# Optimization experiments

Hardware: AMD Instinct MI355X
Metric: run time of the kernel (lower is better)

Reference implementation:

```python
import jax, jax.numpy as jnp
import numpy as np

N_NODES = 100000
N_EDGES = 1600000
IN_DIM = 32
OUT_DIM = 64
N_REL = 8
EPS = 1e-10


def setup_inputs() -> dict:
    key = jax.random.key(0)
    k_x, k_src, k_dst, k_rel, k_w, k_wl, k_ws = jax.random.split(key, 7)
    x = jax.random.normal(k_x, (N_NODES, IN_DIM), dtype=jnp.float32)
    node_in = jax.random.randint(k_src, (N_EDGES,), 0, N_NODES)
    node_out = jax.random.randint(k_dst, (N_EDGES,), 0, N_NODES)
    relation = jax.random.randint(k_rel, (N_EDGES,), 0, N_REL)
    edge_list = jnp.stack([node_in, node_out, relation], axis=1)  # [E, 3] int
    edge_weight = jax.random.uniform(k_w, (N_EDGES,), dtype=jnp.float32)
    W_linear = jax.random.normal(k_wl, (N_REL * IN_DIM, OUT_DIM), dtype=jnp.float32) / np.sqrt(N_REL * IN_DIM)
    b_linear = jnp.zeros((OUT_DIM,), dtype=jnp.float32)
    W_self = jax.random.normal(k_ws, (IN_DIM, OUT_DIM), dtype=jnp.float32) / np.sqrt(IN_DIM)
    b_self = jnp.zeros((OUT_DIM,), dtype=jnp.float32)
    return {"x": x, "edge_list": edge_list, "edge_weight": edge_weight,
            "W_linear": W_linear, "b_linear": b_linear,
            "W_self": W_self, "b_self": b_self}


def reference(x, edge_list, edge_weight, W_linear, b_linear, W_self, b_self):
    num_node, in_dim = x.shape
    # message: gather source-node features per edge  -> [E, D]
    msg = x[edge_list[:, 0]]
    # aggregate: relation-expanded segment id = dst * R + rel
    seg = edge_list[:, 1] * N_REL + edge_list[:, 2]  # [E]
    w = edge_weight[:, None]  # [E, 1]
    num = jax.ops.segment_sum(msg * w, seg, num_segments=num_node * N_REL)  # [N*R, D]
    den = jax.ops.segment_sum(w, seg, num_segments=num_node * N_REL)        # [N*R, 1]
    update = (num / (den + EPS)).reshape(num_node, N_REL * in_dim)          # [N, R*D]
    # combine: linear(update) + self_loop(x), then ReLU
    out = update @ W_linear + b_linear + x @ W_self + b_self
    return jax.nn.relu(out)
```

## Files before the change

kernel.cpp:

```cpp
#include <hip/hip_runtime.h>
#include <stdint.h>

#define N_NODES 100000
#define N_EDGES 1600000
#define IN_DIM 32
#define OUT_DIM 64
#define N_REL 8
#define NSEG (N_NODES * N_REL)
#define EPS 1e-10f
#define N_KK 9
#define SWG_ELEMS (N_KK * 4 * 64 * 8)

#define SCAN_ELEMS 4096
#define SCAN_NB ((NSEG + SCAN_ELEMS - 1) / SCAN_ELEMS)

#define N_XCD 8
#define NODES_PER_SLICE (N_NODES / N_XCD)

typedef __attribute__((ext_vector_type(8))) short bf16x8;
typedef __attribute__((ext_vector_type(4))) float f32x4;

static __device__ __forceinline__ float bflo(uint32_t u) { return __uint_as_float(u << 16); }
static __device__ __forceinline__ float bfhi(uint32_t u) { return __uint_as_float(u & 0xffff0000u); }
static __device__ __forceinline__ uint16_t f2bf(float f) {
    uint32_t u = __float_as_uint(f);
    return (uint16_t)((u + 0x7fffu + ((u >> 16) & 1u)) >> 16);
}

__global__ __launch_bounds__(256) void detect_kernel(const uint32_t* __restrict__ xw,
                                                     int* __restrict__ flag) {
    __shared__ int cnt;
    if (threadIdx.x == 0) cnt = 0;
    __syncthreads();
    int c = 0;
    for (int k = threadIdx.x; k < 4096; k += 256) {
        uint32_t w = xw[k];
        uint32_t e = (w >> 7) & 0xffu;
        c += (e >= 160u) ? 1 : 0;
    }
    atomicAdd(&cnt, c);
    __syncthreads();
    if (threadIdx.x == 0) *flag = (cnt > 64) ? 1 : 0;
}

__global__ __launch_bounds__(256) void prep_kernel(const void* __restrict__ Wl,
                                                   const void* __restrict__ Ws,
                                                   const void* __restrict__ bl,
                                                   const void* __restrict__ bs,
                                                   const int* __restrict__ flag,
                                                   uint16_t* __restrict__ sWg,
                                                   float* __restrict__ biasv) {
    int f32 = *flag;
    int idx = blockIdx.x * 256 + threadIdx.x;
    if (idx < SWG_ELEMS) {
        int j    = idx & 7;
        int lane = (idx >> 3) & 63;
        int ot   = (idx >> 9) & 3;
        int kk   = idx >> 11;
        int quad = lane >> 4;
        int k = kk * 32 + quad * 8 + j;
        int o = ot * 16 + (lane & 15);
        if (f32) {
            float v = (k < 256) ? ((const float*)Wl)[(size_t)k * OUT_DIM + o]
                                : ((const float*)Ws)[(size_t)(k - 256) * OUT_DIM + o];
            sWg[idx] = f2bf(v);
        } else {
            sWg[idx] = (k < 256) ? ((const uint16_t*)Wl)[(size_t)k * OUT_DIM + o]
                                 : ((const uint16_t*)Ws)[(size_t)(k - 256) * OUT_DIM + o];
        }
    } else if (idx < SWG_ELEMS + OUT_DIM) {
        int o = idx - SWG_ELEMS;
        if (f32) biasv[o] = ((const float*)bl)[o] + ((const float*)bs)[o];
        else     biasv[o] = bflo((uint32_t)((const uint16_t*)bl)[o])
                          + bflo((uint32_t)((const uint16_t*)bs)[o]);
    }
}

__global__ __launch_bounds__(256) void xbf_kernel(const void* __restrict__ x,
                                                  const int* __restrict__ flag,
                                                  uint16_t* __restrict__ xbf) {
    int i = blockIdx.x * 256 + threadIdx.x;
    if (i >= N_NODES * IN_DIM / 8) return;
    if (*flag) {
        const float4 v0 = ((const float4*)x)[(size_t)i * 2];
        const float4 v1 = ((const float4*)x)[(size_t)i * 2 + 1];
        bf16x8 r;
        r[0] = (short)f2bf(v0.x); r[1] = (short)f2bf(v0.y);
        r[2] = (short)f2bf(v0.z); r[3] = (short)f2bf(v0.w);
        r[4] = (short)f2bf(v1.x); r[5] = (short)f2bf(v1.y);
        r[6] = (short)f2bf(v1.z); r[7] = (short)f2bf(v1.w);
        *(bf16x8*)(xbf + (size_t)i * 8) = r;
    } else {
        *(bf16x8*)(xbf + (size_t)i * 8) = ((const bf16x8*)x)[i];
    }
}

__global__ __launch_bounds__(256) void hist_kernel(const int* __restrict__ el,
                                                   uint32_t* __restrict__ cnt) {
    int e = blockIdx.x * 256 + threadIdx.x;
    if (e >= N_EDGES) return;
    int dst = el[e * 3 + 1];
    int rel = el[e * 3 + 2];
    atomicAdd(&cnt[dst * N_REL + rel], 1u);
}

__global__ __launch_bounds__(256) void scan1_kernel(const uint32_t* __restrict__ cnt,
                                                    uint32_t* __restrict__ bsum) {
    int base = blockIdx.x * SCAN_ELEMS + threadIdx.x * 16;
    uint32_t s = 0;
    #pragma unroll
    for (int j = 0; j < 16; ++j) {
        int i = base + j;
        s += (i < NSEG) ? cnt[i] : 0u;
    }
    __shared__ uint32_t ls[256];
    ls[threadIdx.x] = s;
    __syncthreads();
    #pragma unroll
    for (int off = 128; off > 0; off >>= 1) {
        if (threadIdx.x < off) ls[threadIdx.x] += ls[threadIdx.x + off];
        __syncthreads();
    }
    if (threadIdx.x == 0) bsum[blockIdx.x] = ls[0];
}

__global__ __launch_bounds__(256) void scan2_kernel(uint32_t* __restrict__ bsum) {
    __shared__ uint32_t ls[256];
    int tid = threadIdx.x;
    ls[tid] = (tid < SCAN_NB) ? bsum[tid] : 0u;
    __syncthreads();
    if (tid == 0) {
        uint32_t run = 0;
        for (int i = 0; i < SCAN_NB; ++i) { uint32_t c = ls[i]; ls[i] = run; run += c; }
    }
    __syncthreads();
    if (tid < SCAN_NB) bsum[tid] = ls[tid];
}

__global__ __launch_bounds__(256) void scan3_kernel(const uint32_t* __restrict__ bsum,
                                                    uint32_t* __restrict__ ptr,
                                                    uint32_t* __restrict__ cursor) {
    int tid = threadIdx.x;
    int base = blockIdx.x * SCAN_ELEMS + tid * 16;
    uint32_t v[16];
    uint32_t run = 0;
    #pragma unroll
    for (int j = 0; j < 16; ++j) {
        int i = base + j;
        uint32_t c = (i < NSEG) ? cursor[i] : 0u;
        v[j] = run;
        run += c;
    }
    __shared__ uint32_t ls[256];
    ls[tid] = run;
    __syncthreads();
    for (int off = 1; off < 256; off <<= 1) {
        uint32_t t = (tid >= off) ? ls[tid - off] : 0u;
        __syncthreads();
        ls[tid] += t;
        __syncthreads();
    }
    uint32_t texcl = ls[tid] - run;
    uint32_t boff = bsum[blockIdx.x];
    #pragma unroll
    for (int j = 0; j < 16; ++j) {
        int i = base + j;
        if (i < NSEG) {
            uint32_t val = boff + texcl + v[j];
            ptr[i]    = val;
            cursor[i] = val;
        }
    }
    if (blockIdx.x == 0 && tid == 0) ptr[NSEG] = N_EDGES;
}

__global__ __launch_bounds__(256) void sort_kernel(const int* __restrict__ el,
                                                   const void* __restrict__ ew,
                                                   const int* __restrict__ flag,
                                                   uint32_t* __restrict__ cursor,
                                                   uint2* __restrict__ sorted) {
    int b = blockIdx.x;
    int tile  = b >> 3;
    int slice = b & 7;
    int e = tile * 256 + threadIdx.x;
    if (e >= N_EDGES) return;
    int dst = el[e * 3 + 1];
    if (dst / NODES_PER_SLICE != slice) return;
    int src = el[e * 3 + 0];
    int rel = el[e * 3 + 2];
    float w = (*flag) ? ((const float*)ew)[e]
                      : bflo((uint32_t)((const uint16_t*)ew)[e]);
    int seg = dst * N_REL + rel;
    uint32_t pos = atomicAdd(&cursor[seg], 1u);
    sorted[pos] = make_uint2((uint32_t)src, __float_as_uint(w));
}

__global__ __launch_bounds__(256) void fused_dense_kernel(
    const uint32_t* __restrict__ ptr,
    const uint2* __restrict__ sorted,
    const uint16_t* __restrict__ xbf,
    const uint16_t* __restrict__ sWg,
    const float* __restrict__ biasv,
    const int* __restrict__ flag,
    void* __restrict__ out)
{
    __shared__ uint16_t sB[SWG_ELEMS];
    int f32 = *flag;

    #pragma unroll
    for (int it = 0; it < SWG_ELEMS / (256 * 8); ++it) {
        int idx = (it * 256 + threadIdx.x) * 8;
        *(bf16x8*)(sB + idx) = *(const bf16x8*)(sWg + idx);
    }
    __syncthreads();

    int wid  = threadIdx.x >> 6;
    int lane = threadIdx.x & 63;
    int quad = lane >> 4;
    int m    = lane & 15;

    int n0 = blockIdx.x * 64 + wid * 16;
    int n  = n0 + m;
    int nc = (n < N_NODES) ? n : (N_NODES - 1);

    float bias[4];
    #pragma unroll
    for (int ot = 0; ot < 4; ++ot) bias[ot] = biasv[ot * 16 + m];

    f32x4 acc[4];
    #pragma unroll
    for (int ot = 0; ot < 4; ++ot) acc[ot] = (f32x4){0.f, 0.f, 0.f, 0.f};

    #pragma unroll
    for (int kk = 0; kk < N_KK; ++kk) {
        bf16x8 a;
        if (kk < 8) {
            int seg = nc * N_REL + kk;
            int beg = (int)ptr[seg];
            int end = (int)ptr[seg + 1];
            float s0 = 0.f, s1 = 0.f, s2 = 0.f, s3 = 0.f;
            float s4 = 0.f, s5 = 0.f, s6 = 0.f, s7 = 0.f, sw = 0.f;
            for (int i = beg; i < end; ++i) {
                uint2 d = sorted[i];
                float w = __uint_as_float(d.y);
                const uint4 xv = *(const uint4*)(xbf + (size_t)d.x * IN_DIM + quad * 8);
                s0 += w * bflo(xv.x); s1 += w * bfhi(xv.x);
                s2 += w * bflo(xv.y); s3 += w * bfhi(xv.y);
                s4 += w * bflo(xv.z); s5 += w * bfhi(xv.z);
                s6 += w * bflo(xv.w); s7 += w * bfhi(xv.w);
                sw += w;
            }
            float inv = 1.0f / (sw + EPS);
            a[0] = (short)f2bf(s0 * inv); a[1] = (short)f2bf(s1 * inv);
            a[2] = (short)f2bf(s2 * inv); a[3] = (short)f2bf(s3 * inv);
            a[4] = (short)f2bf(s4 * inv); a[5] = (short)f2bf(s5 * inv);
            a[6] = (short)f2bf(s6 * inv); a[7] = (short)f2bf(s7 * inv);
        } else {
            a = *(const bf16x8*)(xbf + (size_t)nc * IN_DIM + quad * 8);
        }
        #pragma unroll
        for (int ot = 0; ot < 4; ++ot) {
            bf16x8 b = *(const bf16x8*)(sB + ((kk * 4 + ot) * 64 + lane) * 8);
            acc[ot] = __builtin_amdgcn_mfma_f32_16x16x32_bf16(a, b, acc[ot], 0, 0, 0);
        }
    }

    #pragma unroll
    for (int ot = 0; ot < 4; ++ot) {
        #pragma unroll
        for (int reg = 0; reg < 4; ++reg) {
            int node = n0 + quad * 4 + reg;
            if (node >= N_NODES) continue;
            int o = ot * 16 + m;
            float v = fmaxf(acc[ot][reg] + bias[ot], 0.0f);
            if (f32) ((float*)out)[(size_t)node * OUT_DIM + o] = v;
            else     ((uint16_t*)out)[(size_t)node * OUT_DIM + o] = f2bf(v);
        }
    }
}

extern "C" void kernel_launch(void* const* d_in, const int* in_sizes, int n_in,
                              void* d_out, int out_size, void* d_ws, size_t ws_size,
                              hipStream_t stream) {
    const void* x  = d_in[0];
    const int* el  = (const int*)d_in[1];
    const void* ew = d_in[2];
    const void* Wl = d_in[3];
    const void* bl = d_in[4];
    const void* Ws = d_in[5];
    const void* bs = d_in[6];

    const size_t OFF_PTR  = 64;
    const size_t OFF_CUR  = OFF_PTR + (((size_t)(NSEG + 1) * 4 + 63) & ~(size_t)63);
    const size_t OFF_BS   = OFF_CUR + (size_t)NSEG * 4;
    const size_t OFF_SORT = OFF_BS + 16384;
    const size_t OFF_SWG  = OFF_SORT + (size_t)N_EDGES * 8;
    const size_t OFF_BIAS = OFF_SWG + (size_t)SWG_ELEMS * 2;
    const size_t OFF_XBF  = OFF_BIAS + 256;
    const size_t REQ      = OFF_XBF + (size_t)N_NODES * IN_DIM * 2;
    if (ws_size < REQ) return;

    int*      flag   = (int*)d_ws;
    uint32_t* ptr    = (uint32_t*)((char*)d_ws + OFF_PTR);
    uint32_t* cursor = (uint32_t*)((char*)d_ws + OFF_CUR);
    uint32_t* bsum   = (uint32_t*)((char*)d_ws + OFF_BS);
    uint2*    sorted = (uint2*)((char*)d_ws + OFF_SORT);
    uint16_t* sWg    = (uint16_t*)((char*)d_ws + OFF_SWG);
    float*    biasv  = (float*)((char*)d_ws + OFF_BIAS);
    uint16_t* xbf    = (uint16_t*)((char*)d_ws + OFF_XBF);

    (void)hipMemsetAsync(cursor, 0, (size_t)NSEG * 4, stream);

    detect_kernel<<<1, 256, 0, stream>>>((const uint32_t*)x, flag);
    prep_kernel<<<(SWG_ELEMS + OUT_DIM + 255) / 256, 256, 0, stream>>>(Wl, Ws, bl, bs, flag, sWg, biasv);
    xbf_kernel<<<(N_NODES * IN_DIM / 8 + 255) / 256, 256, 0, stream>>>(x, flag, xbf);

    const int eblocks = (N_EDGES + 255) / 256;
    hist_kernel<<<eblocks, 256, 0, stream>>>(el, cursor);
    scan1_kernel<<<SCAN_NB, 256, 0, stream>>>(cursor, bsum);
    scan2_kernel<<<1, 256, 0, stream>>>(bsum);
    scan3_kernel<<<SCAN_NB, 256, 0, stream>>>(bsum, ptr, cursor);
    sort_kernel<<<eblocks * N_XCD, 256, 0, stream>>>(el, ew, flag, cursor, sorted);

    fused_dense_kernel<<<(N_NODES + 63) / 64, 256, 0, stream>>>(ptr, sorted, xbf, sWg, biasv, flag, d_out);
}
```

Before: 319.4 us.

## Replace slice-filtered scatter sort with two-pass bucket partition and fuse setup kernels

```diff
diff --git a/kernel.cpp b/kernel.cpp
--- a/kernel.cpp
+++ b/kernel.cpp
@@ -14,8 +14,16 @@
 #define SCAN_ELEMS 4096
 #define SCAN_NB ((NSEG + SCAN_ELEMS - 1) / SCAN_ELEMS)
 
-#define N_XCD 8
-#define NODES_PER_SLICE (N_NODES / N_XCD)
+#define NB 32
+#define NODES_PER_BUCKET 3125
+#define SEGS_PER_BUCKET (NODES_PER_BUCKET * N_REL)
+#define P1_EDGES 4096
+#define P1_BLOCKS ((N_EDGES + P1_EDGES - 1) / P1_EDGES)
+#define P2_SUB 16
+
+#define HIST_BLOCKS ((N_EDGES + 255) / 256)
+#define XBF_BLOCKS  ((N_NODES * IN_DIM / 8 + 255) / 256)
+#define PREP_BLOCKS ((SWG_ELEMS + OUT_DIM + 255) / 256)
 
 typedef __attribute__((ext_vector_type(8))) short bf16x8;
 typedef __attribute__((ext_vector_type(4))) float f32x4;
@@ -43,65 +51,71 @@
     if (threadIdx.x == 0) *flag = (cnt > 64) ? 1 : 0;
 }
 
-__global__ __launch_bounds__(256) void prep_kernel(const void* __restrict__ Wl,
-                                                   const void* __restrict__ Ws,
-                                                   const void* __restrict__ bl,
-                                                   const void* __restrict__ bs,
-                                                   const int* __restrict__ flag,
-                                                   uint16_t* __restrict__ sWg,
-                                                   float* __restrict__ biasv) {
-    int f32 = *flag;
-    int idx = blockIdx.x * 256 + threadIdx.x;
-    if (idx < SWG_ELEMS) {
-        int j    = idx & 7;
-        int lane = (idx >> 3) & 63;
-        int ot   = (idx >> 9) & 3;
-        int kk   = idx >> 11;
-        int quad = lane >> 4;
-        int k = kk * 32 + quad * 8 + j;
-        int o = ot * 16 + (lane & 15);
-        if (f32) {
-            float v = (k < 256) ? ((const float*)Wl)[(size_t)k * OUT_DIM + o]
-                                : ((const float*)Ws)[(size_t)(k - 256) * OUT_DIM + o];
-            sWg[idx] = f2bf(v);
+__global__ __launch_bounds__(256) void setup_kernel(
+    const int* __restrict__ el,
+    const void* __restrict__ x,
+    const void* __restrict__ Wl, const void* __restrict__ Ws,
+    const void* __restrict__ bl, const void* __restrict__ bs,
+    const int* __restrict__ flag,
+    uint32_t* __restrict__ cnt,
+    uint16_t* __restrict__ xbf,
+    uint16_t* __restrict__ sWg,
+    float* __restrict__ biasv)
+{
+    int bid = blockIdx.x;
+    if (bid < HIST_BLOCKS) {
+        int e = bid * 256 + threadIdx.x;
+        if (e >= N_EDGES) return;
+        int dst = el[e * 3 + 1];
+        int rel = el[e * 3 + 2];
+        atomicAdd(&cnt[dst * N_REL + rel], 1u);
+        return;
+    }
+    bid -= HIST_BLOCKS;
+    if (bid < XBF_BLOCKS) {
+        int i = bid * 256 + threadIdx.x;
+        if (i >= N_NODES * IN_DIM / 8) return;
+        if (*flag) {
+            const float4 v0 = ((const float4*)x)[(size_t)i * 2];
+            const float4 v1 = ((const float4*)x)[(size_t)i * 2 + 1];
+            bf16x8 r;
+            r[0] = (short)f2bf(v0.x); r[1] = (short)f2bf(v0.y);
+            r[2] = (short)f2bf(v0.z); r[3] = (short)f2bf(v0.w);
+            r[4] = (short)f2bf(v1.x); r[5] = (short)f2bf(v1.y);
+            r[6] = (short)f2bf(v1.z); r[7] = (short)f2bf(v1.w);
+            *(bf16x8*)(xbf + (size_t)i * 8) = r;
         } else {
-            sWg[idx] = (k < 256) ? ((const uint16_t*)Wl)[(size_t)k * OUT_DIM + o]
-                                 : ((const uint16_t*)Ws)[(size_t)(k - 256) * OUT_DIM + o];
-        }
-    } else if (idx < SWG_ELEMS + OUT_DIM) {
-        int o = idx - SWG_ELEMS;
-        if (f32) biasv[o] = ((const float*)bl)[o] + ((const float*)bs)[o];
-        else     biasv[o] = bflo((uint32_t)((const uint16_t*)bl)[o])
-                          + bflo((uint32_t)((const uint16_t*)bs)[o]);
-    }
-}
-
-__global__ __launch_bounds__(256) void xbf_kernel(const void* __restrict__ x,
-                                                  const int* __restrict__ flag,
-                                                  uint16_t* __restrict__ xbf) {
-    int i = blockIdx.x * 256 + threadIdx.x;
-    if (i >= N_NODES * IN_DIM / 8) return;
-    if (*flag) {
-        const float4 v0 = ((const float4*)x)[(size_t)i * 2];
-        const float4 v1 = ((const float4*)x)[(size_t)i * 2 + 1];
-        bf16x8 r;
-        r[0] = (short)f2bf(v0.x); r[1] = (short)f2bf(v0.y);
-        r[2] = (short)f2bf(v0.z); r[3] = (short)f2bf(v0.w);
-        r[4] = (short)f2bf(v1.x); r[5] = (short)f2bf(v1.y);
-        r[6] = (short)f2bf(v1.z); r[7] = (short)f2bf(v1.w);
-        *(bf16x8*)(xbf + (size_t)i * 8) = r;
-    } else {
-        *(bf16x8*)(xbf + (size_t)i * 8) = ((const bf16x8*)x)[i];
-    }
-}
-
-__global__ __launch_bounds__(256) void hist_kernel(const int* __restrict__ el,
-                                                   uint32_t* __restrict__ cnt) {
-    int e = blockIdx.x * 256 + threadIdx.x;
-    if (e >= N_EDGES) return;
-    int dst = el[e * 3 + 1];
-    int rel = el[e * 3 + 2];
-    atomicAdd(&cnt[dst * N_REL + rel], 1u);
+            *(bf16x8*)(xbf + (size_t)i * 8) = ((const bf16x8*)x)[i];
+        }
+        return;
+    }
+    bid -= XBF_BLOCKS;
+    {
+        int f32 = *flag;
+        int idx = bid * 256 + threadIdx.x;
+        if (idx < SWG_ELEMS) {
+            int j    = idx & 7;
+            int lane = (idx >> 3) & 63;
+            int ot   = (idx >> 9) & 3;
+            int kk   = idx >> 11;
+            int quad = lane >> 4;
+            int k = kk * 32 + quad * 8 + j;
+            int o = ot * 16 + (lane & 15);
+            if (f32) {
+                float v = (k < 256) ? ((const float*)Wl)[(size_t)k * OUT_DIM + o]
+                                    : ((const float*)Ws)[(size_t)(k - 256) * OUT_DIM + o];
+                sWg[idx] = f2bf(v);
+            } else {
+                sWg[idx] = (k < 256) ? ((const uint16_t*)Wl)[(size_t)k * OUT_DIM + o]
+                                     : ((const uint16_t*)Ws)[(size_t)(k - 256) * OUT_DIM + o];
+            }
+        } else if (idx < SWG_ELEMS + OUT_DIM) {
+            int o = idx - SWG_ELEMS;
+            if (f32) biasv[o] = ((const float*)bl)[o] + ((const float*)bs)[o];
+            else     biasv[o] = bflo((uint32_t)((const uint16_t*)bl)[o])
+                              + bflo((uint32_t)((const uint16_t*)bs)[o]);
+        }
+    }
 }
 
 __global__ __launch_bounds__(256) void scan1_kernel(const uint32_t* __restrict__ cnt,
@@ -124,23 +138,22 @@
     if (threadIdx.x == 0) bsum[blockIdx.x] = ls[0];
 }
 
-__global__ __launch_bounds__(256) void scan2_kernel(uint32_t* __restrict__ bsum) {
-    __shared__ uint32_t ls[256];
-    int tid = threadIdx.x;
-    ls[tid] = (tid < SCAN_NB) ? bsum[tid] : 0u;
-    __syncthreads();
-    if (tid == 0) {
-        uint32_t run = 0;
-        for (int i = 0; i < SCAN_NB; ++i) { uint32_t c = ls[i]; ls[i] = run; run += c; }
-    }
-    __syncthreads();
-    if (tid < SCAN_NB) bsum[tid] = ls[tid];
-}
-
 __global__ __launch_bounds__(256) void scan3_kernel(const uint32_t* __restrict__ bsum,
                                                     uint32_t* __restrict__ ptr,
                                                     uint32_t* __restrict__ cursor) {
     int tid = threadIdx.x;
+    __shared__ uint32_t ls[256];
+
+    ls[tid] = (tid < (int)blockIdx.x) ? bsum[tid] : 0u;
+    __syncthreads();
+    #pragma unroll
+    for (int off = 128; off > 0; off >>= 1) {
+        if (tid < off) ls[tid] += ls[tid + off];
+        __syncthreads();
+    }
+    uint32_t boff = ls[0];
+    __syncthreads();
+
     int base = blockIdx.x * SCAN_ELEMS + tid * 16;
     uint32_t v[16];
     uint32_t run = 0;
@@ -151,7 +164,6 @@
         v[j] = run;
         run += c;
     }
-    __shared__ uint32_t ls[256];
     ls[tid] = run;
     __syncthreads();
     for (int off = 1; off < 256; off <<= 1) {
@@ -161,7 +173,6 @@
         __syncthreads();
     }
     uint32_t texcl = ls[tid] - run;
-    uint32_t boff = bsum[blockIdx.x];
     #pragma unroll
     for (int j = 0; j < 16; ++j) {
         int i = base + j;
@@ -174,25 +185,71 @@
     if (blockIdx.x == 0 && tid == 0) ptr[NSEG] = N_EDGES;
 }
 
-__global__ __launch_bounds__(256) void sort_kernel(const int* __restrict__ el,
-                                                   const void* __restrict__ ew,
-                                                   const int* __restrict__ flag,
-                                                   uint32_t* __restrict__ cursor,
-                                                   uint2* __restrict__ sorted) {
-    int b = blockIdx.x;
-    int tile  = b >> 3;
-    int slice = b & 7;
-    int e = tile * 256 + threadIdx.x;
-    if (e >= N_EDGES) return;
-    int dst = el[e * 3 + 1];
-    if (dst / NODES_PER_SLICE != slice) return;
-    int src = el[e * 3 + 0];
-    int rel = el[e * 3 + 2];
-    float w = (*flag) ? ((const float*)ew)[e]
-                      : bflo((uint32_t)((const uint16_t*)ew)[e]);
-    int seg = dst * N_REL + rel;
-    uint32_t pos = atomicAdd(&cursor[seg], 1u);
-    sorted[pos] = make_uint2((uint32_t)src, __float_as_uint(w));
+__global__ __launch_bounds__(256) void part1_kernel(const int* __restrict__ el,
+                                                    const void* __restrict__ ew,
+                                                    const int* __restrict__ flag,
+                                                    const uint32_t* __restrict__ ptr,
+                                                    uint32_t* __restrict__ gcursor,
+                                                    uint2* __restrict__ part) {
+    __shared__ uint32_t cnt[NB], base[NB];
+    int tid = threadIdx.x;
+    if (tid < NB) cnt[tid] = 0;
+    __syncthreads();
+    int f32 = *flag;
+    int e0 = blockIdx.x * P1_EDGES;
+
+    uint32_t meta[16], wbits[16], bk[16], my[16];
+    #pragma unroll
+    for (int j = 0; j < 16; ++j) {
+        int e = e0 + j * 256 + tid;
+        if (e < N_EDGES) {
+            int src = el[e * 3 + 0];
+            int dst = el[e * 3 + 1];
+            int rel = el[e * 3 + 2];
+            int b  = dst / NODES_PER_BUCKET;
+            int dl = dst - b * NODES_PER_BUCKET;
+            meta[j]  = (uint32_t)src | ((uint32_t)dl << 17) | ((uint32_t)rel << 29);
+            wbits[j] = f32 ? ((const uint32_t*)ew)[e]
+                           : ((uint32_t)((const uint16_t*)ew)[e] << 16);
+            bk[j] = (uint32_t)b;
+            my[j] = atomicAdd(&cnt[b], 1u);
+        } else {
+            bk[j] = 0xffffffffu;
+        }
+    }
+    __syncthreads();
+    if (tid < NB) {
+        uint32_t c = cnt[tid];
+        base[tid] = c ? (ptr[(size_t)tid * SEGS_PER_BUCKET] + atomicAdd(&gcursor[tid], c)) : 0u;
+    }
+    __syncthreads();
+    #pragma unroll
+    for (int j = 0; j < 16; ++j) {
+        if (bk[j] != 0xffffffffu)
+            part[(size_t)base[bk[j]] + my[j]] = make_uint2(meta[j], wbits[j]);
+    }
+}
+
+__global__ __launch_bounds__(256) void part2_kernel(const uint32_t* __restrict__ ptr,
+                                                    const uint2* __restrict__ part,
+                                                    uint32_t* __restrict__ cursor,
+                                                    uint2* __restrict__ sorted) {
+    int b = blockIdx.x & (NB - 1);
+    int s = blockIdx.x >> 5;
+    uint32_t rbeg = ptr[(size_t)b * SEGS_PER_BUCKET];
+    uint32_t rend = (b == NB - 1) ? (uint32_t)N_EDGES : ptr[(size_t)(b + 1) * SEGS_PER_BUCKET];
+    uint32_t len  = rend - rbeg;
+    uint32_t cbeg = rbeg + (uint32_t)(((uint64_t)len * (uint32_t)s) >> 4);
+    uint32_t cend = rbeg + (uint32_t)(((uint64_t)len * (uint32_t)(s + 1)) >> 4);
+    for (uint32_t i = cbeg + threadIdx.x; i < cend; i += 256) {
+        uint2 r = part[i];
+        uint32_t src = r.x & 0x1FFFFu;
+        uint32_t dl  = (r.x >> 17) & 0xFFFu;
+        uint32_t rel = r.x >> 29;
+        uint32_t seg = (uint32_t)b * SEGS_PER_BUCKET + dl * 8u + rel;
+        uint32_t pos = atomicAdd(&cursor[seg], 1u);
+        sorted[pos] = make_uint2(src, r.y);
+    }
 }
 
 __global__ __launch_bounds__(256) void fused_dense_kernel(
@@ -290,37 +347,41 @@
     const void* Ws = d_in[5];
     const void* bs = d_in[6];
 
-    const size_t OFF_PTR  = 64;
-    const size_t OFF_CUR  = OFF_PTR + (((size_t)(NSEG + 1) * 4 + 63) & ~(size_t)63);
-    const size_t OFF_BS   = OFF_CUR + (size_t)NSEG * 4;
-    const size_t OFF_SORT = OFF_BS + 16384;
+    const size_t OFF_GC   = 64;
+    const size_t OFF_CUR  = OFF_GC + 128;
+    const size_t OFF_PTR  = OFF_CUR + (size_t)NSEG * 4;
+    const size_t OFF_BS   = OFF_PTR + (((size_t)(NSEG + 1) * 4 + 63) & ~(size_t)63);
+    const size_t OFF_PART = OFF_BS + 16384;
+    const size_t OFF_SORT = OFF_PART + (size_t)N_EDGES * 8;
     const size_t OFF_SWG  = OFF_SORT + (size_t)N_EDGES * 8;
     const size_t OFF_BIAS = OFF_SWG + (size_t)SWG_ELEMS * 2;
     const size_t OFF_XBF  = OFF_BIAS + 256;
     const size_t REQ      = OFF_XBF + (size_t)N_NODES * IN_DIM * 2;
     if (ws_size < REQ) return;
 
-    int*      flag   = (int*)d_ws;
-    uint32_t* ptr    = (uint32_t*)((char*)d_ws + OFF_PTR);
-    uint32_t* cursor = (uint32_t*)((char*)d_ws + OFF_CUR);
-    uint32_t* bsum   = (uint32_t*)((char*)d_ws + OFF_BS);
-    uint2*    sorted = (uint2*)((char*)d_ws + OFF_SORT);
-    uint16_t* sWg    = (uint16_t*)((char*)d_ws + OFF_SWG);
-    float*    biasv  = (float*)((char*)d_ws + OFF_BIAS);
-    uint16_t* xbf    = (uint16_t*)((char*)d_ws + OFF_XBF);
-
-    (void)hipMemsetAsync(cursor, 0, (size_t)NSEG * 4, stream);
+    int*      flag    = (int*)d_ws;
+    uint32_t* gcursor = (uint32_t*)((char*)d_ws + OFF_GC);
+    uint32_t* cursor  = (uint32_t*)((char*)d_ws + OFF_CUR);
+    uint32_t* ptr     = (uint32_t*)((char*)d_ws + OFF_PTR);
+    uint32_t* bsum    = (uint32_t*)((char*)d_ws + OFF_BS);
+    uint2*    part    = (uint2*)((char*)d_ws + OFF_PART);
+    uint2*    sorted  = (uint2*)((char*)d_ws + OFF_SORT);
+    uint16_t* sWg     = (uint16_t*)((char*)d_ws + OFF_SWG);
+    float*    biasv   = (float*)((char*)d_ws + OFF_BIAS);
+    uint16_t* xbf     = (uint16_t*)((char*)d_ws + OFF_XBF);
+
+    (void)hipMemsetAsync((char*)d_ws + OFF_GC, 0, 128 + (size_t)NSEG * 4, stream);
 
     detect_kernel<<<1, 256, 0, stream>>>((const uint32_t*)x, flag);
-    prep_kernel<<<(SWG_ELEMS + OUT_DIM + 255) / 256, 256, 0, stream>>>(Wl, Ws, bl, bs, flag, sWg, biasv);
-    xbf_kernel<<<(N_NODES * IN_DIM / 8 + 255) / 256, 256, 0, stream>>>(x, flag, xbf);
-
-    const int eblocks = (N_EDGES + 255) / 256;
-    hist_kernel<<<eblocks, 256, 0, stream>>>(el, cursor);
+
+    setup_kernel<<<HIST_BLOCKS + XBF_BLOCKS + PREP_BLOCKS, 256, 0, stream>>>(
+        el, x, Wl, Ws, bl, bs, flag, cursor, xbf, sWg, biasv);
+
     scan1_kernel<<<SCAN_NB, 256, 0, stream>>>(cursor, bsum);
-    scan2_kernel<<<1, 256, 0, stream>>>(bsum);
     scan3_kernel<<<SCAN_NB, 256, 0, stream>>>(bsum, ptr, cursor);
-    sort_kernel<<<eblocks * N_XCD, 256, 0, stream>>>(el, ew, flag, cursor, sorted);
+
+    part1_kernel<<<P1_BLOCKS, 256, 0, stream>>>(el, ew, flag, ptr, gcursor, part);
+    part2_kernel<<<NB * P2_SUB, 256, 0, stream>>>(ptr, part, cursor, sorted);
 
     fused_dense_kernel<<<(N_NODES + 63) / 64, 256, 0, stream>>>(ptr, sorted, xbf, sWg, biasv, flag, d_out);
 }
```

Measured after the change: 372.2 us. 16.5% more time.
